# Performance work log

Hardware: AMD Instinct MI355X
Metric: run time of the kernel (lower is better)

The kernel has to match this reference:

```python
import jax, jax.numpy as jnp
import numpy as np

H, DK, DV, MID, DM = 8, 64, 64, 128, 512
GN_EPS = 1e-5

def _xavier(k, fi, fo):
    lim = float(np.sqrt(6.0 / (fi + fo)))
    return jax.random.uniform(k, (fi, fo), minval=-lim, maxval=lim, dtype=jnp.float32)

def setup_inputs() -> dict:
    key = jax.random.key(0)
    ks = jax.random.split(key, 16)
    bs, nq, nk = 8, 100, 100
    z = lambda n: jnp.zeros((n,), jnp.float32)
    o = lambda n: jnp.ones((n,), jnp.float32)
    return {
        'queries': jax.random.normal(ks[0], (bs, nq, DM), jnp.float32),
        'keys':    jax.random.normal(ks[1], (bs, nk, DM), jnp.float32),
        'values':  jax.random.normal(ks[2], (bs, nk, DM), jnp.float32),
        'W_q1': _xavier(ks[3], DM, H * DK), 'b_q1': z(H * DK), 'g_q1w': o(H * DK), 'g_q1b': z(H * DK),
        'W_q2': _xavier(ks[4], DM, H * DV), 'b_q2': z(H * DV), 'g_q2w': o(H * DV), 'g_q2b': z(H * DV),
        'W_k':  _xavier(ks[5], DM, H * DK), 'b_k':  z(H * DK), 'g_kw':  o(H * DK), 'g_kb':  z(H * DK),
        'W_v':  _xavier(ks[6], DM, H * DV), 'b_v':  z(H * DV), 'g_vw':  o(H * DV), 'g_vb':  z(H * DV),
        'W_m': _xavier(ks[7], DK, MID), 'b_m': z(MID),
        'W_s': _xavier(ks[8], MID, 1),  'b_s': z(1),
        'W_c': _xavier(ks[9], MID, DV), 'b_c': z(DV),
        'W_o': _xavier(ks[10], H * DV, DM), 'b_o': z(DM),
    }

def _in_proj(x, W, b, gw, gb, dg):
    # Linear -> ELU -> GroupNorm(h groups) over flattened (bs*n, h*dg)
    y = jax.nn.elu(x @ W + b)                     # (N, h*dg)
    yg = y.reshape(-1, H, dg)                     # per-sample groups
    mu = yg.mean(-1, keepdims=True)
    var = yg.var(-1, keepdims=True)
    yg = (yg - mu) * jax.lax.rsqrt(var + GN_EPS)
    return yg.reshape(-1, H * dg) * gw + gb

def reference(queries, keys, values,
              W_q1, b_q1, g_q1w, g_q1b, W_q2, b_q2, g_q2w, g_q2b,
              W_k, b_k, g_kw, g_kb, W_v, b_v, g_vw, g_vb,
              W_m, b_m, W_s, b_s, W_c, b_c, W_o, b_o):
    bs, nq, _ = queries.shape
    nk = keys.shape[1]
    q_flat = queries.reshape(bs * nq, DM)
    k_flat = keys.reshape(bs * nk, DM)
    v_flat = values.reshape(bs * nk, DM)
    q1 = _in_proj(q_flat, W_q1, b_q1, g_q1w, g_q1b, DK).reshape(bs, nq, H, DK).transpose(0, 2, 1, 3)
    q2 = _in_proj(q_flat, W_q2, b_q2, g_q2w, g_q2b, DV).reshape(bs, nq, H, DV).transpose(0, 2, 1, 3)
    k  = _in_proj(k_flat, W_k,  b_k,  g_kw,  g_kb,  DK).reshape(bs, nk, H, DK).transpose(0, 2, 1, 3)
    v  = _in_proj(v_flat, W_v,  b_v,  g_vw,  g_vb,  DV).reshape(bs, nk, H, DV).transpose(0, 2, 1, 3)
    # outer elementwise product feature map: (bs,h,nq,nk,dk)
    prod = q1[:, :, :, None, :] * k[:, :, None, :, :]
    attn_map = jax.nn.relu(jnp.einsum('bhqkd,dm->bhqkm', prod, W_m) + b_m)  # (bs,h,nq,nk,mid)
    attn_spatial = jnp.einsum('bhqkm,m->bhqk', attn_map, W_s[:, 0]) + b_s[0]
    attn_spatial = jax.nn.softmax(attn_spatial, axis=-1)
    att_map_pool = attn_map.mean(axis=3)                                    # (bs,h,nq,mid)
    attn_channel = jax.nn.sigmoid(att_map_pool @ W_c + b_c)                 # (bs,h,nq,dv)
    attn_v = jnp.einsum('bhqk,bhkd->bhqd', attn_spatial, v) * q2 * attn_channel
    out = attn_v.transpose(0, 2, 1, 3).reshape(bs, nq, H * DV) @ W_o + b_o
    return out
```

## Files before the change

### kernel.cpp

```cpp
#include <hip/hip_runtime.h>
#include <hip/hip_bf16.h>
#include <math.h>

#define NH 8
#define DMv 512
#define BSv 8
#define NQv 100
#define NKv 100

typedef __attribute__((ext_vector_type(8))) short short8;
typedef __attribute__((ext_vector_type(4))) float f32x4;

__device__ __forceinline__ unsigned short bf16u(float f) {
    __hip_bfloat16 h = __float2bfloat16(f);
    return *(unsigned short*)&h;
}
__device__ __forceinline__ unsigned int pkbf(float lo, float hi) {
    return ((unsigned int)bf16u(hi) << 16) | (unsigned int)bf16u(lo);
}

__global__ __launch_bounds__(256) void wt_kernel(
    const float* __restrict__ W_q1, const float* __restrict__ W_q2,
    const float* __restrict__ W_k,  const float* __restrict__ W_v,
    const float* __restrict__ W_o,  const float* __restrict__ Wc,
    unsigned short* __restrict__ wt, unsigned int* __restrict__ wcp)
{
    __shared__ float tile[64][68];
    const int z = blockIdx.z;
    const int t = threadIdx.x;
    if (z == 5) {
        if (blockIdx.x != 0 || blockIdx.y != 0) return;
        for (int i = t; i < 4096; i += 256) {
            const int m2 = i >> 6, d = i & 63;
            wcp[i] = pkbf(Wc[(size_t)(2 * m2) * 64 + d], Wc[(size_t)(2 * m2 + 1) * 64 + d]);
        }
        return;
    }
    const float* W = (z == 0) ? W_q1 : (z == 1) ? W_q2 : (z == 2) ? W_k : (z == 3) ? W_v : W_o;
    unsigned short* out = wt + (size_t)z * 512 * 512;
    const int k0 = blockIdx.x * 64, n0 = blockIdx.y * 64;
    const int r = t >> 2, c = t & 3;
#pragma unroll
    for (int i = 0; i < 4; i++) {
        float4 v = *(const float4*)&W[(size_t)(k0 + r) * 512 + n0 + c * 16 + i * 4];
        *(float4*)&tile[r][c * 16 + i * 4] = v;
    }
    __syncthreads();
#pragma unroll
    for (int jj = 0; jj < 4; jj++) {
        const int kb = c * 16 + jj * 4;
        ushort4 u;
        u.x = bf16u(tile[kb + 0][r]); u.y = bf16u(tile[kb + 1][r]);
        u.z = bf16u(tile[kb + 2][r]); u.w = bf16u(tile[kb + 3][r]);
        *(ushort4*)&out[(size_t)(n0 + r) * 512 + k0 + kb] = u;
    }
}

__global__ __launch_bounds__(256) void proj_kernel(
    const float* __restrict__ xq, const float* __restrict__ xk, const float* __restrict__ xv,
    const unsigned short* __restrict__ wt,
    const float* __restrict__ bq1, const float* __restrict__ gq1w, const float* __restrict__ gq1b,
    const float* __restrict__ bq2, const float* __restrict__ gq2w, const float* __restrict__ gq2b,
    const float* __restrict__ bk,  const float* __restrict__ gkw,  const float* __restrict__ gkb,
    const float* __restrict__ bv,  const float* __restrict__ gvw,  const float* __restrict__ gvb,
    float* __restrict__ q1o, float* __restrict__ q2o, float* __restrict__ ko, float* __restrict__ vo)
{
    __shared__ char A_s[64 * 144];
    __shared__ char B_s[64 * 144];
    __shared__ float Y_s[64][68];

    const int p = blockIdx.z;
    const float *x, *bb, *gw, *gb;
    float* o;
    if (p == 0)      { x = xq; bb = bq1; gw = gq1w; gb = gq1b; o = q1o; }
    else if (p == 1) { x = xq; bb = bq2; gw = gq2w; gb = gq2b; o = q2o; }
    else if (p == 2) { x = xk; bb = bk;  gw = gkw;  gb = gkb;  o = ko;  }
    else             { x = xv; bb = bv;  gw = gvw;  gb = gvb;  o = vo;  }
    const unsigned short* WT = wt + (size_t)p * 512 * 512;

    const int t = threadIdx.x;
    const int r0 = blockIdx.x * 64;
    const int ct = blockIdx.y;

    const int lane = t & 63, wave = t >> 6;
    const int wr = wave >> 1, wc = wave & 1;
    const int lr = lane & 15, lq = lane >> 4;
    const int srow = t >> 2, sc = t & 3;

    f32x4 acc[2][2];
#pragma unroll
    for (int i = 0; i < 2; i++)
#pragma unroll
        for (int j = 0; j < 2; j++) acc[i][j] = (f32x4){0.f, 0.f, 0.f, 0.f};

    const int arow = (r0 + srow < 800) ? (r0 + srow) : 799;

    for (int kk = 0; kk < 8; kk++) {
        const int k0 = kk * 64;
#pragma unroll
        for (int uu = 0; uu < 2; uu++) {
            const int u = sc * 2 + uu;
            float4 f0 = *(const float4*)&x[(size_t)arow * 512 + k0 + u * 8];
            float4 f1 = *(const float4*)&x[(size_t)arow * 512 + k0 + u * 8 + 4];
            uint4 w;
            w.x = pkbf(f0.x, f0.y); w.y = pkbf(f0.z, f0.w);
            w.z = pkbf(f1.x, f1.y); w.w = pkbf(f1.z, f1.w);
            *(uint4*)(A_s + srow * 144 + u * 16) = w;
        }
#pragma unroll
        for (int uu = 0; uu < 2; uu++) {
            const int u = sc * 2 + uu;
            uint4 w = *(const uint4*)((const char*)(WT + (size_t)(ct * 64 + srow) * 512 + k0) + u * 16);
            *(uint4*)(B_s + srow * 144 + u * 16) = w;
        }
        __syncthreads();
#pragma unroll
        for (int ks = 0; ks < 2; ks++) {
            short8 a0 = *(const short8*)(A_s + (wr * 32 + lr) * 144 + (ks * 4 + lq) * 16);
            short8 a1 = *(const short8*)(A_s + (wr * 32 + 16 + lr) * 144 + (ks * 4 + lq) * 16);
            short8 b0 = *(const short8*)(B_s + (wc * 32 + lr) * 144 + (ks * 4 + lq) * 16);
            short8 b1 = *(const short8*)(B_s + (wc * 32 + 16 + lr) * 144 + (ks * 4 + lq) * 16);
            acc[0][0] = __builtin_amdgcn_mfma_f32_16x16x32_bf16(a0, b0, acc[0][0], 0, 0, 0);
            acc[0][1] = __builtin_amdgcn_mfma_f32_16x16x32_bf16(a0, b1, acc[0][1], 0, 0, 0);
            acc[1][0] = __builtin_amdgcn_mfma_f32_16x16x32_bf16(a1, b0, acc[1][0], 0, 0, 0);
            acc[1][1] = __builtin_amdgcn_mfma_f32_16x16x32_bf16(a1, b1, acc[1][1], 0, 0, 0);
        }
        __syncthreads();
    }

#pragma unroll
    for (int nt = 0; nt < 2; nt++) {
        const int colL = wc * 32 + nt * 16 + lr;
        const float bias = bb[ct * 64 + colL];
#pragma unroll
        for (int mt = 0; mt < 2; mt++) {
#pragma unroll
            for (int r = 0; r < 4; r++) {
                const int row = wr * 32 + mt * 16 + lq * 4 + r;
                float y = acc[mt][nt][r] + bias;
                y = (y > 0.f) ? y : expm1f(y);
                Y_s[row][colL] = y;
            }
        }
    }
    __syncthreads();

    {
        const int row = t >> 2, c = t & 3;
        float v[16];
        float s = 0.f, ss = 0.f;
#pragma unroll
        for (int i = 0; i < 16; i++) {
            v[i] = Y_s[row][c * 16 + i];
            s += v[i]; ss += v[i] * v[i];
        }
        s += __shfl_xor(s, 1); ss += __shfl_xor(ss, 1);
        s += __shfl_xor(s, 2); ss += __shfl_xor(ss, 2);
        const float mu = s * (1.f / 64.f);
        const float var = ss * (1.f / 64.f) - mu * mu;
        const float rs = 1.0f / sqrtf(var + 1e-5f);
        const int rowg = r0 + row;
        if (rowg < 800) {
            const int b = rowg / 100, sq = rowg % 100;
            const size_t base = (((size_t)(b * NH + ct) * NQv) + sq) * 64 + c * 16;
            const int j0 = ct * 64 + c * 16;
#pragma unroll
            for (int i4 = 0; i4 < 4; i4++) {
                float4 gwv = *(const float4*)&gw[j0 + i4 * 4];
                float4 gbv = *(const float4*)&gb[j0 + i4 * 4];
                float4 ov;
                ov.x = (v[i4 * 4 + 0] - mu) * rs * gwv.x + gbv.x;
                ov.y = (v[i4 * 4 + 1] - mu) * rs * gwv.y + gbv.y;
                ov.z = (v[i4 * 4 + 2] - mu) * rs * gwv.z + gbv.z;
                ov.w = (v[i4 * 4 + 3] - mu) * rs * gwv.w + gbv.w;
                *(float4*)&o[base + i4 * 4] = ov;
            }
        }
    }
}

__global__ __launch_bounds__(512) void attn_kernel(
    const float* __restrict__ q1g, const float* __restrict__ q2g,
    const float* __restrict__ kg, const float* __restrict__ vg,
    const float* __restrict__ Wm, const float* __restrict__ bm,
    const float* __restrict__ Ws, const float* __restrict__ bs_,
    const unsigned int* __restrict__ wcp, const float* __restrict__ bc,
    float* __restrict__ attn_v)
{
    __shared__ unsigned short Wm_s[8192];
    __shared__ unsigned short K_s[6400];
    __shared__ unsigned int  V_pk[3200];
    __shared__ float2 bmws_s[128];
    __shared__ float p_ws[8][128];
    __shared__ float pool_ws[8][128];
    __shared__ float lg_ws[8][112];

    const int t = threadIdx.x;
    const int qt = blockIdx.x;
    const int bh = blockIdx.y;
    const int q0 = qt * 25;

    const float* Kg = kg + (size_t)bh * NKv * 64;
    const float* Vg = vg + (size_t)bh * NKv * 64;

    for (int i = t; i < 800; i += 512) {
        const int k = i >> 3, u = i & 7;
        float4 a = *(const float4*)(Kg + k * 64 + u * 8);
        float4 b = *(const float4*)(Kg + k * 64 + u * 8 + 4);
        uint4 w;
        w.x = pkbf(a.x, a.y); w.y = pkbf(a.z, a.w);
        w.z = pkbf(b.x, b.y); w.w = pkbf(b.z, b.w);
        *(uint4*)((char*)K_s + k * 128 + ((u ^ (k & 7)) * 16)) = w;
    }
    for (int i = t; i < 1024; i += 512) {
        const int u = i >> 7, m = i & 127;
        float f[8];
#pragma unroll
        for (int j = 0; j < 8; j++) f[j] = Wm[(size_t)(u * 8 + j) * 128 + m];
        uint4 w;
        w.x = pkbf(f[0], f[1]); w.y = pkbf(f[2], f[3]);
        w.z = pkbf(f[4], f[5]); w.w = pkbf(f[6], f[7]);
        *(uint4*)((char*)Wm_s + m * 128 + ((u ^ (m & 7)) * 16)) = w;
    }
    for (int i = t; i < 800; i += 512) {
        const int k2 = i >> 4, du = i & 15;
        float4 a = *(const float4*)(Vg + (size_t)(2 * k2) * 64 + du * 4);
        float4 b = *(const float4*)(Vg + (size_t)(2 * k2 + 1) * 64 + du * 4);
        uint4 w;
        w.x = pkbf(a.x, b.x); w.y = pkbf(a.y, b.y);
        w.z = pkbf(a.z, b.z); w.w = pkbf(a.w, b.w);
        *(uint4*)(V_pk + k2 * 64 + du * 4) = w;
    }
    if (t < 128) bmws_s[t] = make_float2(bm[t], Ws[t]);
    const float bsv = bs_[0];
    __syncthreads();

    const int wv = t >> 6, lane = t & 63;
    const int lr = lane & 15, lq = lane >> 4;
    float* p_w = p_ws[wv];
    float* pool_w = pool_ws[wv];
    float* lg_w = lg_ws[wv];
    const int d = lane;
    const int b_ = bh >> 3, hh = bh & 7;
    const float bcd = bc[d];
    const float km6 = (lr < 4) ? 1.f : 0.f;

    for (int qi = wv; qi < 25; qi += 8) {
        const int q = q0 + qi;
        const size_t qb = ((size_t)bh * NQv + q) * 64;

        float q1v[2][8];
#pragma unroll
        for (int ks = 0; ks < 2; ks++) {
            float4 x = *(const float4*)(q1g + qb + ks * 32 + lq * 8);
            float4 y = *(const float4*)(q1g + qb + ks * 32 + lq * 8 + 4);
            q1v[ks][0] = x.x; q1v[ks][1] = x.y; q1v[ks][2] = x.z; q1v[ks][3] = x.w;
            q1v[ks][4] = y.x; q1v[ks][5] = y.y; q1v[ks][6] = y.z; q1v[ks][7] = y.w;
        }

        float pool_acc[8][4];
#pragma unroll
        for (int mt = 0; mt < 8; mt++)
#pragma unroll
            for (int r = 0; r < 4; r++) pool_acc[mt][r] = 0.f;

#pragma unroll 1
        for (int kt = 0; kt < 7; kt++) {
            const int k = kt * 16 + lr;
            const int kr = (k < 100) ? k : 99;
            const float km = (kt < 6) ? 1.f : km6;

            uint4 bfr0, bfr1;
#pragma unroll
            for (int ks = 0; ks < 2; ks++) {
                const int uu = ks * 4 + lq;
                uint4 Ka = *(const uint4*)((const char*)K_s + kr * 128 + ((uu ^ (kr & 7)) * 16));
                uint4 w;
#pragma unroll
                for (int j = 0; j < 4; j++) {
                    const unsigned int u0 = ((const unsigned int*)&Ka)[j];
                    const float klo = __uint_as_float(u0 << 16);
                    const float khi = __uint_as_float(u0 & 0xffff0000u);
                    ((unsigned int*)&w)[j] = pkbf(klo * q1v[ks][2 * j], khi * q1v[ks][2 * j + 1]);
                }
                if (ks == 0) bfr0 = w; else bfr1 = w;
            }

            float lgA = 0.f, lgB = 0.f;
#pragma unroll
            for (int mt = 0; mt < 8; mt++) {
                int m = mt * 16 + lr;
                asm volatile("" : "+v"(m));
                const char* wrow = (const char*)Wm_s + m * 128;
                short8 afr0 = *(const short8*)(wrow + ((lq ^ (m & 7)) * 16));
                short8 afr1 = *(const short8*)(wrow + (((4 + lq) ^ (m & 7)) * 16));
                f32x4 acc = (f32x4){0.f, 0.f, 0.f, 0.f};
                acc = __builtin_amdgcn_mfma_f32_16x16x32_bf16(afr0, *(const short8*)&bfr0, acc, 0, 0, 0);
                acc = __builtin_amdgcn_mfma_f32_16x16x32_bf16(afr1, *(const short8*)&bfr1, acc, 0, 0, 0);
                const float2* bw = &bmws_s[(m - lr) + lq * 4];
                float4 bwa = *(const float4*)(bw);
                float4 bwb = *(const float4*)(bw + 2);
                const float v0 = fmaxf(acc[0] + bwa.x, 0.f);
                const float v1 = fmaxf(acc[1] + bwa.z, 0.f);
                const float v2 = fmaxf(acc[2] + bwb.x, 0.f);
                const float v3 = fmaxf(acc[3] + bwb.z, 0.f);
                lgA = fmaf(bwa.y, v0, lgA); lgA = fmaf(bwa.w, v1, lgA);
                lgB = fmaf(bwb.y, v2, lgB); lgB = fmaf(bwb.w, v3, lgB);
                pool_acc[mt][0] = fmaf(v0, km, pool_acc[mt][0]);
                pool_acc[mt][1] = fmaf(v1, km, pool_acc[mt][1]);
                pool_acc[mt][2] = fmaf(v2, km, pool_acc[mt][2]);
                pool_acc[mt][3] = fmaf(v3, km, pool_acc[mt][3]);
            }
            float lg = lgA + lgB;
            lg += __shfl_xor(lg, 16);
            lg += __shfl_xor(lg, 32);
            if (lq == 0) lg_w[kt * 16 + lr] = lg + bsv;
        }

#pragma unroll
        for (int mt = 0; mt < 8; mt++) {
#pragma unroll
            for (int r = 0; r < 4; r++) {
                pool_acc[mt][r] += __shfl_xor(pool_acc[mt][r], 1);
                pool_acc[mt][r] += __shfl_xor(pool_acc[mt][r], 2);
                pool_acc[mt][r] += __shfl_xor(pool_acc[mt][r], 4);
                pool_acc[mt][r] += __shfl_xor(pool_acc[mt][r], 8);
            }
            if (lr == 0)
                *(float4*)&pool_w[mt * 16 + lq * 4] = make_float4(
                    pool_acc[mt][0] * 0.01f, pool_acc[mt][1] * 0.01f,
                    pool_acc[mt][2] * 0.01f, pool_acc[mt][3] * 0.01f);
        }

        float lg[7];
#pragma unroll
        for (int kt = 0; kt < 7; kt++) lg[kt] = lg_w[kt * 16 + lr];
        float mx = -3.0e38f;
#pragma unroll
        for (int kt = 0; kt < 6; kt++) mx = fmaxf(mx, lg[kt]);
        if (lr < 4) mx = fmaxf(mx, lg[6]);
        mx = fmaxf(mx, __shfl_xor(mx, 1));
        mx = fmaxf(mx, __shfl_xor(mx, 2));
        mx = fmaxf(mx, __shfl_xor(mx, 4));
        mx = fmaxf(mx, __shfl_xor(mx, 8));
        float e[7];
        float sm = 0.f;
#pragma unroll
        for (int kt = 0; kt < 7; kt++) {
            const bool valid = (kt < 6) | (lr < 4);
            e[kt] = valid ? __expf(lg[kt] - mx) : 0.f;
            sm += e[kt];
        }
        sm += __shfl_xor(sm, 1);
        sm += __shfl_xor(sm, 2);
        sm += __shfl_xor(sm, 4);
        sm += __shfl_xor(sm, 8);
        const float inv = 1.f / sm;
        if (lq == 0) {
#pragma unroll
            for (int kt = 0; kt < 7; kt++) p_w[kt * 16 + lr] = e[kt] * inv;
        }

        float sva = 0.f, svb = 0.f;
        for (int k2 = 0; k2 < 50; k2++) {
            const float2 pp = *(const float2*)&p_w[2 * k2];
            const unsigned int vp = V_pk[k2 * 64 + d];
            sva = fmaf(pp.x, __uint_as_float(vp << 16), sva);
            svb = fmaf(pp.y, __uint_as_float(vp & 0xffff0000u), svb);
        }
        float cha = 0.f, chb = 0.f;
        for (int m2 = 0; m2 < 64; m2++) {
            const float2 pl = *(const float2*)&pool_w[2 * m2];
            const unsigned int wp = wcp[m2 * 64 + d];
            cha = fmaf(pl.x, __uint_as_float(wp << 16), cha);
            chb = fmaf(pl.y, __uint_as_float(wp & 0xffff0000u), chb);
        }
        const float ch = 1.f / (1.f + __expf(-((cha + chb) + bcd)));
        const float ov = (sva + svb) * q2g[qb + d] * ch;
        attn_v[(((size_t)(b_ * NQv + q) * NH) + hh) * 64 + d] = ov;
    }
}

__global__ __launch_bounds__(256) void out_proj_kernel(
    const float* __restrict__ x, const unsigned short* __restrict__ WT,
    const float* __restrict__ bo, float* __restrict__ out)
{
    __shared__ char A_s[64 * 144];
    __shared__ char B_s[64 * 144];

    const int t = threadIdx.x;
    const int r0 = blockIdx.x * 64;
    const int ct = blockIdx.y;

    const int lane = t & 63, wave = t >> 6;
    const int wr = wave >> 1, wc = wave & 1;
    const int lr = lane & 15, lq = lane >> 4;
    const int srow = t >> 2, sc = t & 3;

    f32x4 acc[2][2];
#pragma unroll
    for (int i = 0; i < 2; i++)
#pragma unroll
        for (int j = 0; j < 2; j++) acc[i][j] = (f32x4){0.f, 0.f, 0.f, 0.f};

    const int arow = (r0 + srow < 800) ? (r0 + srow) : 799;

    for (int kk = 0; kk < 8; kk++) {
        const int k0 = kk * 64;
#pragma unroll
        for (int uu = 0; uu < 2; uu++) {
            const int u = sc * 2 + uu;
            float4 f0 = *(const float4*)&x[(size_t)arow * 512 + k0 + u * 8];
            float4 f1 = *(const float4*)&x[(size_t)arow * 512 + k0 + u * 8 + 4];
            uint4 w;
            w.x = pkbf(f0.x, f0.y); w.y = pkbf(f0.z, f0.w);
            w.z = pkbf(f1.x, f1.y); w.w = pkbf(f1.z, f1.w);
            *(uint4*)(A_s + srow * 144 + u * 16) = w;
        }
#pragma unroll
        for (int uu = 0; uu < 2; uu++) {
            const int u = sc * 2 + uu;
            uint4 w = *(const uint4*)((const char*)(WT + (size_t)(ct * 64 + srow) * 512 + k0) + u * 16);
            *(uint4*)(B_s + srow * 144 + u * 16) = w;
        }
        __syncthreads();
#pragma unroll
        for (int ks = 0; ks < 2; ks++) {
            short8 a0 = *(const short8*)(A_s + (wr * 32 + lr) * 144 + (ks * 4 + lq) * 16);
            short8 a1 = *(const short8*)(A_s + (wr * 32 + 16 + lr) * 144 + (ks * 4 + lq) * 16);
            short8 b0 = *(const short8*)(B_s + (wc * 32 + lr) * 144 + (ks * 4 + lq) * 16);
            short8 b1 = *(const short8*)(B_s + (wc * 32 + 16 + lr) * 144 + (ks * 4 + lq) * 16);
            acc[0][0] = __builtin_amdgcn_mfma_f32_16x16x32_bf16(a0, b0, acc[0][0], 0, 0, 0);
            acc[0][1] = __builtin_amdgcn_mfma_f32_16x16x32_bf16(a0, b1, acc[0][1], 0, 0, 0);
            acc[1][0] = __builtin_amdgcn_mfma_f32_16x16x32_bf16(a1, b0, acc[1][0], 0, 0, 0);
            acc[1][1] = __builtin_amdgcn_mfma_f32_16x16x32_bf16(a1, b1, acc[1][1], 0, 0, 0);
        }
        __syncthreads();
    }

#pragma unroll
    for (int nt = 0; nt < 2; nt++) {
        const int j = ct * 64 + wc * 32 + nt * 16 + lr;
        const float bias = bo[j];
#pragma unroll
        for (int mt = 0; mt < 2; mt++) {
#pragma unroll
            for (int r = 0; r < 4; r++) {
                const int rowg = r0 + wr * 32 + mt * 16 + lq * 4 + r;
                if (rowg < 800) out[(size_t)rowg * 512 + j] = acc[mt][nt][r] + bias;
            }
        }
    }
}

extern "C" void kernel_launch(void* const* d_in, const int* in_sizes, int n_in,
                              void* d_out, int out_size, void* d_ws, size_t ws_size,
                              hipStream_t stream) {
    (void)in_sizes; (void)n_in; (void)out_size; (void)ws_size;
    const float* queries = (const float*)d_in[0];
    const float* keys    = (const float*)d_in[1];
    const float* values  = (const float*)d_in[2];
    const float* W_q1 = (const float*)d_in[3];
    const float* b_q1 = (const float*)d_in[4];
    const float* g_q1w = (const float*)d_in[5];
    const float* g_q1b = (const float*)d_in[6];
    const float* W_q2 = (const float*)d_in[7];
    const float* b_q2 = (const float*)d_in[8];
    const float* g_q2w = (const float*)d_in[9];
    const float* g_q2b = (const float*)d_in[10];
    const float* W_k = (const float*)d_in[11];
    const float* b_k = (const float*)d_in[12];
    const float* g_kw = (const float*)d_in[13];
    const float* g_kb = (const float*)d_in[14];
    const float* W_v = (const float*)d_in[15];
    const float* b_v = (const float*)d_in[16];
    const float* g_vw = (const float*)d_in[17];
    const float* g_vb = (const float*)d_in[18];
    const float* W_m = (const float*)d_in[19];
    const float* b_m = (const float*)d_in[20];
    const float* W_s = (const float*)d_in[21];
    const float* b_s = (const float*)d_in[22];
    const float* W_c = (const float*)d_in[23];
    const float* b_c = (const float*)d_in[24];
    const float* W_o = (const float*)d_in[25];
    const float* b_o = (const float*)d_in[26];

    float* ws = (float*)d_ws;
    const size_t PROJ = (size_t)BSv * NQv * 512;
    float* q1 = ws;
    float* q2 = q1 + PROJ;
    float* kk = q2 + PROJ;
    float* vv = kk + PROJ;
    float* av = vv + PROJ;
    unsigned short* wt = (unsigned short*)(av + PROJ);
    unsigned int* wcp = (unsigned int*)(wt + (size_t)5 * 512 * 512);

    wt_kernel<<<dim3(8, 8, 6), 256, 0, stream>>>(W_q1, W_q2, W_k, W_v, W_o, W_c, wt, wcp);

    proj_kernel<<<dim3(13, 8, 4), 256, 0, stream>>>(
        queries, keys, values, wt,
        b_q1, g_q1w, g_q1b,
        b_q2, g_q2w, g_q2b,
        b_k, g_kw, g_kb,
        b_v, g_vw, g_vb,
        q1, q2, kk, vv);

    attn_kernel<<<dim3(4, BSv * NH), 512, 0, stream>>>(
        q1, q2, kk, vv, W_m, b_m, W_s, b_s, wcp, b_c, av);

    out_proj_kernel<<<dim3(13, 8), 256, 0, stream>>>(av, wt + (size_t)4 * 512 * 512, b_o, (float*)d_out);
}
```

Before: 93.82 us.

## Restructure attention score loop to reuse Wm fragments across key tiles

Replaces the runtime loop over 7 key tiles, which reloaded all Wm and bias fragments from LDS for every tile, with two fully unrolled halves of 4 and 3 key tiles. In each half the Wm fragments and bias/Ws values are loaded once per m-tile and reused across all key tiles in that half. The intent is to cut LDS traffic and give the scheduler more independent MFMAs to interleave. In exchange, register pressure rises because of multiple B fragments and logit accumulators, and q1 is reloaded from global memory once per half.

```diff
diff --git a/kernel.cpp b/kernel.cpp
--- a/kernel.cpp
+++ b/kernel.cpp
@@ -176,6 +176,85 @@
                 *(float4*)&o[base + i4 * 4] = ov;
             }
         }
+    }
+}
+
+template<int KTBASE, int NKT>
+__device__ __forceinline__ void s_phase_half(
+    const unsigned short* K_s, const unsigned short* Wm_s, const float2* bmws_s,
+    const float* q1ptr, int lr, int lq, float km6,
+    float pool_acc[8][4], float* lg_w, float bsv)
+{
+    float q1v[2][8];
+#pragma unroll
+    for (int ks = 0; ks < 2; ks++) {
+        float4 x = *(const float4*)(q1ptr + ks * 32 + lq * 8);
+        float4 y = *(const float4*)(q1ptr + ks * 32 + lq * 8 + 4);
+        q1v[ks][0] = x.x; q1v[ks][1] = x.y; q1v[ks][2] = x.z; q1v[ks][3] = x.w;
+        q1v[ks][4] = y.x; q1v[ks][5] = y.y; q1v[ks][6] = y.z; q1v[ks][7] = y.w;
+    }
+    uint4 bfr[NKT][2];
+#pragma unroll
+    for (int kk2 = 0; kk2 < NKT; kk2++) {
+        const int kt = KTBASE + kk2;
+        const int k = kt * 16 + lr;
+        const int kr = (k < 100) ? k : 99;
+#pragma unroll
+        for (int ks = 0; ks < 2; ks++) {
+            const int uu = ks * 4 + lq;
+            uint4 Ka = *(const uint4*)((const char*)K_s + kr * 128 + ((uu ^ (kr & 7)) * 16));
+            uint4 w;
+#pragma unroll
+            for (int j = 0; j < 4; j++) {
+                const unsigned int u0 = ((const unsigned int*)&Ka)[j];
+                const float klo = __uint_as_float(u0 << 16);
+                const float khi = __uint_as_float(u0 & 0xffff0000u);
+                ((unsigned int*)&w)[j] = pkbf(klo * q1v[ks][2 * j], khi * q1v[ks][2 * j + 1]);
+            }
+            bfr[kk2][ks] = w;
+        }
+    }
+    float lgacc[NKT];
+#pragma unroll
+    for (int kk2 = 0; kk2 < NKT; kk2++) lgacc[kk2] = 0.f;
+
+#pragma unroll
+    for (int mt = 0; mt < 8; mt++) {
+        int m = mt * 16 + lr;
+        asm volatile("" : "+v"(m));
+        const char* wrow = (const char*)Wm_s + m * 128;
+        short8 afr0 = *(const short8*)(wrow + ((lq ^ (m & 7)) * 16));
+        short8 afr1 = *(const short8*)(wrow + (((4 + lq) ^ (m & 7)) * 16));
+        const float2* bw = &bmws_s[(m - lr) + lq * 4];
+        float4 bwa = *(const float4*)(bw);
+        float4 bwb = *(const float4*)(bw + 2);
+#pragma unroll
+        for (int kk2 = 0; kk2 < NKT; kk2++) {
+            const int kt = KTBASE + kk2;
+            const float km = (kt < 6) ? 1.f : km6;
+            f32x4 acc = (f32x4){0.f, 0.f, 0.f, 0.f};
+            acc = __builtin_amdgcn_mfma_f32_16x16x32_bf16(afr0, *(const short8*)&bfr[kk2][0], acc, 0, 0, 0);
+            acc = __builtin_amdgcn_mfma_f32_16x16x32_bf16(afr1, *(const short8*)&bfr[kk2][1], acc, 0, 0, 0);
+            const float v0 = fmaxf(acc[0] + bwa.x, 0.f);
+            const float v1 = fmaxf(acc[1] + bwa.z, 0.f);
+            const float v2 = fmaxf(acc[2] + bwb.x, 0.f);
+            const float v3 = fmaxf(acc[3] + bwb.z, 0.f);
+            lgacc[kk2] = fmaf(bwa.y, v0, lgacc[kk2]);
+            lgacc[kk2] = fmaf(bwa.w, v1, lgacc[kk2]);
+            lgacc[kk2] = fmaf(bwb.y, v2, lgacc[kk2]);
+            lgacc[kk2] = fmaf(bwb.w, v3, lgacc[kk2]);
+            pool_acc[mt][0] = fmaf(v0, km, pool_acc[mt][0]);
+            pool_acc[mt][1] = fmaf(v1, km, pool_acc[mt][1]);
+            pool_acc[mt][2] = fmaf(v2, km, pool_acc[mt][2]);
+            pool_acc[mt][3] = fmaf(v3, km, pool_acc[mt][3]);
+        }
+    }
+#pragma unroll
+    for (int kk2 = 0; kk2 < NKT; kk2++) {
+        float lg = lgacc[kk2];
+        lg += __shfl_xor(lg, 16);
+        lg += __shfl_xor(lg, 32);
+        if (lq == 0) lg_w[(KTBASE + kk2) * 16 + lr] = lg + bsv;
     }
 }
 
@@ -249,73 +328,14 @@
         const int q = q0 + qi;
         const size_t qb = ((size_t)bh * NQv + q) * 64;
 
-        float q1v[2][8];
-#pragma unroll
-        for (int ks = 0; ks < 2; ks++) {
-            float4 x = *(const float4*)(q1g + qb + ks * 32 + lq * 8);
-            float4 y = *(const float4*)(q1g + qb + ks * 32 + lq * 8 + 4);
-            q1v[ks][0] = x.x; q1v[ks][1] = x.y; q1v[ks][2] = x.z; q1v[ks][3] = x.w;
-            q1v[ks][4] = y.x; q1v[ks][5] = y.y; q1v[ks][6] = y.z; q1v[ks][7] = y.w;
-        }
-
         float pool_acc[8][4];
 #pragma unroll
         for (int mt = 0; mt < 8; mt++)
 #pragma unroll
             for (int r = 0; r < 4; r++) pool_acc[mt][r] = 0.f;
 
-#pragma unroll 1
-        for (int kt = 0; kt < 7; kt++) {
-            const int k = kt * 16 + lr;
-            const int kr = (k < 100) ? k : 99;
-            const float km = (kt < 6) ? 1.f : km6;
-
-            uint4 bfr0, bfr1;
-#pragma unroll
-            for (int ks = 0; ks < 2; ks++) {
-                const int uu = ks * 4 + lq;
-                uint4 Ka = *(const uint4*)((const char*)K_s + kr * 128 + ((uu ^ (kr & 7)) * 16));
-                uint4 w;
-#pragma unroll
-                for (int j = 0; j < 4; j++) {
-                    const unsigned int u0 = ((const unsigned int*)&Ka)[j];
-                    const float klo = __uint_as_float(u0 << 16);
-                    const float khi = __uint_as_float(u0 & 0xffff0000u);
-                    ((unsigned int*)&w)[j] = pkbf(klo * q1v[ks][2 * j], khi * q1v[ks][2 * j + 1]);
-                }
-                if (ks == 0) bfr0 = w; else bfr1 = w;
-            }
-
-            float lgA = 0.f, lgB = 0.f;
-#pragma unroll
-            for (int mt = 0; mt < 8; mt++) {
-                int m = mt * 16 + lr;
-                asm volatile("" : "+v"(m));
-                const char* wrow = (const char*)Wm_s + m * 128;
-                short8 afr0 = *(const short8*)(wrow + ((lq ^ (m & 7)) * 16));
-                short8 afr1 = *(const short8*)(wrow + (((4 + lq) ^ (m & 7)) * 16));
-                f32x4 acc = (f32x4){0.f, 0.f, 0.f, 0.f};
-                acc = __builtin_amdgcn_mfma_f32_16x16x32_bf16(afr0, *(const short8*)&bfr0, acc, 0, 0, 0);
-                acc = __builtin_amdgcn_mfma_f32_16x16x32_bf16(afr1, *(const short8*)&bfr1, acc, 0, 0, 0);
-                const float2* bw = &bmws_s[(m - lr) + lq * 4];
-                float4 bwa = *(const float4*)(bw);
-                float4 bwb = *(const float4*)(bw + 2);
-                const float v0 = fmaxf(acc[0] + bwa.x, 0.f);
-                const float v1 = fmaxf(acc[1] + bwa.z, 0.f);
-                const float v2 = fmaxf(acc[2] + bwb.x, 0.f);
-                const float v3 = fmaxf(acc[3] + bwb.z, 0.f);
-                lgA = fmaf(bwa.y, v0, lgA); lgA = fmaf(bwa.w, v1, lgA);
-                lgB = fmaf(bwb.y, v2, lgB); lgB = fmaf(bwb.w, v3, lgB);
-                pool_acc[mt][0] = fmaf(v0, km, pool_acc[mt][0]);
-                pool_acc[mt][1] = fmaf(v1, km, pool_acc[mt][1]);
-                pool_acc[mt][2] = fmaf(v2, km, pool_acc[mt][2]);
-                pool_acc[mt][3] = fmaf(v3, km, pool_acc[mt][3]);
-            }
-            float lg = lgA + lgB;
-            lg += __shfl_xor(lg, 16);
-            lg += __shfl_xor(lg, 32);
-            if (lq == 0) lg_w[kt * 16 + lr] = lg + bsv;
-        }
+        s_phase_half<0, 4>(K_s, Wm_s, bmws_s, q1g + qb, lr, lq, km6, pool_acc, lg_w, bsv);
+        s_phase_half<4, 3>(K_s, Wm_s, bmws_s, q1g + qb, lr, lq, km6, pool_acc, lg_w, bsv);
 
 #pragma unroll
         for (int mt = 0; mt < 8; mt++) {
```

New measurement: 174.7 us. 86.3% more time.
